# Optimization experiments

Hardware: AMD Instinct MI355X
Metric: run time of the kernel (lower is better)

The kernel has to match this reference:

```python
import jax, jax.numpy as jnp
import numpy as np

N = 50000          # nodes
E = 1600000        # edges (avg degree 32)
NUM_FEAT = 512
HIDDEN = 128
NUM_CLASS = 40
NUM_LAYERS = 4
EPS = 0.3


def setup_inputs() -> dict:
    key = jax.random.key(0)
    ks = jax.random.split(key, 8)
    x = jax.random.normal(ks[0], (N, NUM_FEAT), dtype=jnp.float32)
    edge_index = jax.random.randint(ks[1], (2, E), 0, N, dtype=jnp.int64)
    gain = 1.414  # xavier_normal_(gain=1.414) as in reset_parameters
    W1 = jax.random.normal(ks[2], (HIDDEN, NUM_FEAT), dtype=jnp.float32) * gain * (2.0 / (HIDDEN + NUM_FEAT)) ** 0.5
    b1 = jnp.zeros((HIDDEN,), dtype=jnp.float32)
    W2 = jax.random.normal(ks[3], (NUM_CLASS, HIDDEN), dtype=jnp.float32) * gain * (2.0 / (NUM_CLASS + HIDDEN)) ** 0.5
    b2 = jnp.zeros((NUM_CLASS,), dtype=jnp.float32)
    # FAConv attention vectors: Linear(channels, 1, bias=False) per layer
    att_l = jax.random.normal(ks[4], (NUM_LAYERS, HIDDEN), dtype=jnp.float32) * (2.0 / (1 + HIDDEN)) ** 0.5
    att_r = jax.random.normal(ks[5], (NUM_LAYERS, HIDDEN), dtype=jnp.float32) * (2.0 / (1 + HIDDEN)) ** 0.5
    return dict(x=x, edge_index=edge_index, W1=W1, b1=b1, W2=W2, b2=b2, att_l=att_l, att_r=att_r)


def reference(x, edge_index, W1, b1, W2, b2, att_l, att_r):
    n = x.shape[0]
    # gcn_norm with self-loops (FAConv default add_self_loops=True)
    loops = jnp.arange(n, dtype=edge_index.dtype)
    src = jnp.concatenate([edge_index[0], loops])  # source j
    dst = jnp.concatenate([edge_index[1], loops])  # target i
    deg = jax.ops.segment_sum(jnp.ones_like(src, dtype=x.dtype), dst, num_segments=n)
    dis = jax.lax.rsqrt(jnp.maximum(deg, 1.0))
    norm = dis[src] * dis[dst]  # [E+N]

    # eval mode: dropout is identity
    h = jax.nn.relu(x @ W1.T + b1)  # [N, HIDDEN]
    raw = h
    for l in range(NUM_LAYERS):
        al = h @ att_l[l]  # [N]
        ar = h @ att_r[l]  # [N]
        coef = jnp.tanh(al[src] + ar[dst]) * norm            # [E+N]
        agg = jax.ops.segment_sum(h[src] * coef[:, None], dst, num_segments=n)
        h = agg + EPS * raw
    logits = h @ W2.T + b2  # [N, NUM_CLASS]
    return jax.nn.log_softmax(logits, axis=1)
```

## Files before the change

### kernel.cpp

```cpp
#include <hip/hip_runtime.h>
#include <cmath>


#define HIDDEN 128
#define FEAT 512
#define NCLASS 40
#define LDST 40
#define LDSW 132
#define NB 256
#define PITCH 12544
#define BM1 64

typedef __attribute__((ext_vector_type(8))) short short8;
typedef __attribute__((ext_vector_type(4))) float f32x4;

__device__ __forceinline__ float bf_lo(unsigned u) { return __uint_as_float(u << 16); }
__device__ __forceinline__ float bf_hi(unsigned u) { return __uint_as_float(u & 0xffff0000u); }
__device__ __forceinline__ unsigned pack_bf16(float x, float y) {
    unsigned ux = __float_as_uint(x);
    unsigned uy = __float_as_uint(y);
    unsigned lx = (ux + 0x7fffu + ((ux >> 16) & 1u)) >> 16;
    unsigned hy = (uy + 0x7fffu + ((uy >> 16) & 1u)) & 0xffff0000u;
    return hy | lx;
}
__device__ __forceinline__ float fast_tanh(float x) {
    x = fminf(fmaxf(x, -15.f), 15.f);
    float e = __expf(2.f * x);
    return (e - 1.f) / (e + 1.f);
}

__global__ __launch_bounds__(256) void k_hist(const int* __restrict__ ei, int E, int CE,
                                              unsigned* __restrict__ partial,
                                              ushort* __restrict__ lrank) {
    __shared__ unsigned lh[PITCH];
    const int b = blockIdx.x, tid = threadIdx.x;
    for (int w = tid; w < PITCH; w += 256) lh[w] = 0;
    __syncthreads();
    int e0 = b * CE, e1 = min(E, e0 + CE);
    for (int e = e0 + tid; e < e1; e += 256) {
        int dst = ei[E + e];
        int sh = (dst & 3) * 8;
        unsigned old = atomicAdd(&lh[dst >> 2], 1u << sh);
        lrank[e] = (ushort)((old >> sh) & 0xffu);
    }
    __syncthreads();
    unsigned* prow = partial + (size_t)b * PITCH;
    for (int w = tid; w < PITCH; w += 256) prow[w] = lh[w];
}

__global__ __launch_bounds__(256) void k_hscan(unsigned* __restrict__ partial,
                                               int* __restrict__ deg,
                                               float* __restrict__ dis, int n) {
    int w = blockIdx.x * 256 + threadIdx.x;
    if (w >= PITCH) return;
    unsigned run = 0;
    size_t idx = w;
    for (int b = 0; b < NB; ++b, idx += PITCH) {
        unsigned v = partial[idx];
        partial[idx] = run;
        run += v;
    }
    int node = 4 * w;
    int d0 = run & 0xffu, d1 = (run >> 8) & 0xffu, d2 = (run >> 16) & 0xffu, d3 = run >> 24;
    if (node < n)     { deg[node]     = d0; dis[node]     = rsqrtf((float)(d0 + 1)); }
    if (node + 1 < n) { deg[node + 1] = d1; dis[node + 1] = rsqrtf((float)(d1 + 1)); }
    if (node + 2 < n) { deg[node + 2] = d2; dis[node + 2] = rsqrtf((float)(d2 + 1)); }
    if (node + 3 < n) { deg[node + 3] = d3; dis[node + 3] = rsqrtf((float)(d3 + 1)); }
}

__global__ __launch_bounds__(256) void k_scan1(const int* __restrict__ deg, int* __restrict__ offs,
                                               int* __restrict__ part, int n) {
    __shared__ int s[256];
    int tid = threadIdx.x;
    int gid = blockIdx.x * 256 + tid;
    int v = (gid < n) ? deg[gid] : 0;
    s[tid] = v;
    __syncthreads();
    for (int off = 1; off < 256; off <<= 1) {
        int t = (tid >= off) ? s[tid - off] : 0;
        __syncthreads();
        s[tid] += t;
        __syncthreads();
    }
    if (gid < n) offs[gid] = s[tid] - v;
    if (tid == 255) part[blockIdx.x] = s[255];
}

__global__ __launch_bounds__(256) void k_scan2(int* __restrict__ part, int nb) {
    __shared__ int s[256];
    int tid = threadIdx.x;
    int v = (tid < nb) ? part[tid] : 0;
    s[tid] = v;
    __syncthreads();
    for (int off = 1; off < 256; off <<= 1) {
        int t = (tid >= off) ? s[tid - off] : 0;
        __syncthreads();
        s[tid] += t;
        __syncthreads();
    }
    if (tid < nb) part[tid] = s[tid] - v;
}

__global__ __launch_bounds__(256) void k_scan3(int* __restrict__ offs, const int* __restrict__ part,
                                               int n, int E) {
    int gid = blockIdx.x * 256 + threadIdx.x;
    if (gid < n) offs[gid] += part[blockIdx.x];
    if (gid == 0) offs[n] = E;
}

__global__ __launch_bounds__(256) void k_csr_fill(const int* __restrict__ ei, int E, int CE,
                                                  const int* __restrict__ offs,
                                                  const unsigned* __restrict__ partial,
                                                  const ushort* __restrict__ lrank,
                                                  int* __restrict__ csrc) {
    __shared__ unsigned lp[PITCH];
    const int b = blockIdx.x, tid = threadIdx.x;
    const unsigned* prow = partial + (size_t)b * PITCH;
    for (int w = tid; w < PITCH; w += 256) lp[w] = prow[w];
    __syncthreads();
    int e0 = b * CE, e1 = min(E, e0 + CE);
    for (int e = e0 + tid; e < e1; e += 256) {
        int dst = ei[E + e];
        int src = ei[e];
        unsigned wv = lp[dst >> 2];
        int base = (wv >> ((dst & 3) * 8)) & 0xffu;
        csrc[offs[dst] + base + (int)lrank[e]] = src;
    }
}

__global__ __launch_bounds__(256) void k_gemm1(const float* __restrict__ x,
                                               const float* __restrict__ W1,
                                               const float* __restrict__ b1,
                                               float* __restrict__ h, int M) {
    __shared__ ushort As[BM1 * LDST];
    __shared__ ushort Bs[128 * LDST];
    const int tid = threadIdx.x;
    const int bm = blockIdx.x * BM1;
    const int wave = tid >> 6, lane = tid & 63;
    const int rh = (wave >> 1) * 32;
    const int ch = (wave & 1) * 64;
    const int sub = lane & 15, quad = lane >> 4;
    const int lrow = tid >> 3;
    const int lcol = (tid & 7) * 4;
    f32x4 acc[2][4] = {};
    float4 av[2], bv[4];
#pragma unroll
    for (int i = 0; i < 2; ++i) {
        int grow = bm + lrow + 32 * i;
        av[i] = (grow < M) ? *(const float4*)(x + (size_t)grow * FEAT + lcol)
                           : make_float4(0.f, 0.f, 0.f, 0.f);
    }
#pragma unroll
    for (int i = 0; i < 4; ++i)
        bv[i] = *(const float4*)(W1 + (size_t)(lrow + 32 * i) * FEAT + lcol);

    for (int k0 = 0; k0 < FEAT; k0 += 32) {
#pragma unroll
        for (int i = 0; i < 2; ++i)
            *(uint2*)(As + (lrow + 32 * i) * LDST + lcol) =
                make_uint2(pack_bf16(av[i].x, av[i].y), pack_bf16(av[i].z, av[i].w));
#pragma unroll
        for (int i = 0; i < 4; ++i)
            *(uint2*)(Bs + (lrow + 32 * i) * LDST + lcol) =
                make_uint2(pack_bf16(bv[i].x, bv[i].y), pack_bf16(bv[i].z, bv[i].w));
        __syncthreads();
        if (k0 + 32 < FEAT) {
            const int kn = k0 + 32;
#pragma unroll
            for (int i = 0; i < 2; ++i) {
                int grow = bm + lrow + 32 * i;
                av[i] = (grow < M) ? *(const float4*)(x + (size_t)grow * FEAT + kn + lcol)
                                   : make_float4(0.f, 0.f, 0.f, 0.f);
            }
#pragma unroll
            for (int i = 0; i < 4; ++i)
                bv[i] = *(const float4*)(W1 + (size_t)(lrow + 32 * i) * FEAT + kn + lcol);
        }
        short8 af[2], bfr[4];
#pragma unroll
        for (int t = 0; t < 2; ++t)
            af[t] = *(const short8*)(As + (rh + t * 16 + sub) * LDST + quad * 8);
#pragma unroll
        for (int u = 0; u < 4; ++u)
            bfr[u] = *(const short8*)(Bs + (ch + u * 16 + sub) * LDST + quad * 8);
#pragma unroll
        for (int t = 0; t < 2; ++t)
#pragma unroll
            for (int u = 0; u < 4; ++u)
                acc[t][u] = __builtin_amdgcn_mfma_f32_16x16x32_bf16(af[t], bfr[u], acc[t][u], 0, 0, 0);
        __syncthreads();
    }
    float b1v[4];
#pragma unroll
    for (int u = 0; u < 4; ++u) b1v[u] = b1[ch + u * 16 + sub];
#pragma unroll
    for (int t = 0; t < 2; ++t) {
#pragma unroll
        for (int u = 0; u < 4; ++u) {
            int col = ch + u * 16 + sub;
#pragma unroll
            for (int r2 = 0; r2 < 4; ++r2) {
                int grow = bm + rh + t * 16 + quad * 4 + r2;
                if (grow < M)
                    h[(size_t)grow * HIDDEN + col] = fmaxf(acc[t][u][r2] + b1v[u], 0.f);
            }
        }
    }
}

__global__ __launch_bounds__(256) void k_prep(const float* __restrict__ h, unsigned* __restrict__ hbf,
                       const float* __restrict__ attl, const float* __restrict__ attr,
                       const float* __restrict__ dis, float2* __restrict__ al2,
                       float* __restrict__ ar, int n) {
    int node = (blockIdx.x * blockDim.x + threadIdx.x) >> 6;
    int lane = threadIdx.x & 63;
    if (node >= n) return;
    float2 hv = ((const float2*)(h + (size_t)node * HIDDEN))[lane];
    hbf[(size_t)node * 64 + lane] = pack_bf16(hv.x, hv.y);
    float pl = hv.x * attl[2 * lane] + hv.y * attl[2 * lane + 1];
    float pr = hv.x * attr[2 * lane] + hv.y * attr[2 * lane + 1];
    for (int off = 32; off; off >>= 1) {
        pl += __shfl_down(pl, off);
        pr += __shfl_down(pr, off);
    }
    if (lane == 0) {
        al2[node] = make_float2(pl, dis[node]);
        ar[node] = pr;
    }
}

__global__ __launch_bounds__(256) void k_aggregate(
                            const unsigned* __restrict__ hbf, const float* __restrict__ raw,
                            const float2* __restrict__ al2, const float* __restrict__ ar,
                            const int* __restrict__ offs, const int* __restrict__ csrc,
                            float* __restrict__ hout, unsigned* __restrict__ houtbf,
                            const float* __restrict__ attl_n, const float* __restrict__ attr_n,
                            float2* __restrict__ al2_o, float* __restrict__ ar_o, int n) {
    int node = (blockIdx.x * blockDim.x + threadIdx.x) >> 6;
    int lane = threadIdx.x & 63;
    if (node >= n) return;
    const int grp = lane >> 4;
    const int sub = lane & 15;
    const float arn = ar[node];
    const float2 selfld = al2[node];
    const float disn = selfld.y;
    float acc[8] = {0.f, 0.f, 0.f, 0.f, 0.f, 0.f, 0.f, 0.f};
    int e0 = offs[node], e1 = offs[node + 1];
    for (int base = e0; base < e1; base += 64) {
        int cnt = min(64, e1 - base);
        int idx = base + lane;
        int smy = (lane < cnt) ? csrc[idx] : node;
        float2 lmy = al2[smy];
        float cmy = (lane < cnt) ? fast_tanh(lmy.x + arn) * lmy.y * disn : 0.f;
        int t = 0;
        for (; t + 16 <= cnt; t += 16) {
            int sa = __shfl(smy, t + grp);
            int sb = __shfl(smy, t + 4 + grp);
            int sc = __shfl(smy, t + 8 + grp);
            int sd = __shfl(smy, t + 12 + grp);
            float ca = __shfl(cmy, t + grp);
            float cb = __shfl(cmy, t + 4 + grp);
            float cc = __shfl(cmy, t + 8 + grp);
            float cd = __shfl(cmy, t + 12 + grp);
            uint4 ra = *(const uint4*)(hbf + (size_t)sa * 64 + sub * 4);
            uint4 rb = *(const uint4*)(hbf + (size_t)sb * 64 + sub * 4);
            uint4 rc = *(const uint4*)(hbf + (size_t)sc * 64 + sub * 4);
            uint4 rd = *(const uint4*)(hbf + (size_t)sd * 64 + sub * 4);
            acc[0] += ca * bf_lo(ra.x); acc[1] += ca * bf_hi(ra.x);
            acc[2] += ca * bf_lo(ra.y); acc[3] += ca * bf_hi(ra.y);
            acc[4] += ca * bf_lo(ra.z); acc[5] += ca * bf_hi(ra.z);
            acc[6] += ca * bf_lo(ra.w); acc[7] += ca * bf_hi(ra.w);
            acc[0] += cb * bf_lo(rb.x); acc[1] += cb * bf_hi(rb.x);
            acc[2] += cb * bf_lo(rb.y); acc[3] += cb * bf_hi(rb.y);
            acc[4] += cb * bf_lo(rb.z); acc[5] += cb * bf_hi(rb.z);
            acc[6] += cb * bf_lo(rb.w); acc[7] += cb * bf_hi(rb.w);
            acc[0] += cc * bf_lo(rc.x); acc[1] += cc * bf_hi(rc.x);
            acc[2] += cc * bf_lo(rc.y); acc[3] += cc * bf_hi(rc.y);
            acc[4] += cc * bf_lo(rc.z); acc[5] += cc * bf_hi(rc.z);
            acc[6] += cc * bf_lo(rc.w); acc[7] += cc * bf_hi(rc.w);
            acc[0] += cd * bf_lo(rd.x); acc[1] += cd * bf_hi(rd.x);
            acc[2] += cd * bf_lo(rd.y); acc[3] += cd * bf_hi(rd.y);
            acc[4] += cd * bf_lo(rd.z); acc[5] += cd * bf_hi(rd.z);
            acc[6] += cd * bf_lo(rd.w); acc[7] += cd * bf_hi(rd.w);
        }
        for (; t < cnt; t += 4) {
            int sa = __shfl(smy, t + grp);
            float ca = __shfl(cmy, t + grp);
            uint4 ra = *(const uint4*)(hbf + (size_t)sa * 64 + sub * 4);
            acc[0] += ca * bf_lo(ra.x); acc[1] += ca * bf_hi(ra.x);
            acc[2] += ca * bf_lo(ra.y); acc[3] += ca * bf_hi(ra.y);
            acc[4] += ca * bf_lo(ra.z); acc[5] += ca * bf_hi(ra.z);
            acc[6] += ca * bf_lo(ra.w); acc[7] += ca * bf_hi(ra.w);
        }
    }
#pragma unroll
    for (int j = 0; j < 8; ++j) {
        acc[j] += __shfl_xor(acc[j], 16);
        acc[j] += __shfl_xor(acc[j], 32);
    }
    {
        float c = fast_tanh(selfld.x + arn) * disn * disn;
        uint4 r = *(const uint4*)(hbf + (size_t)node * 64 + sub * 4);
        acc[0] += c * bf_lo(r.x); acc[1] += c * bf_hi(r.x);
        acc[2] += c * bf_lo(r.y); acc[3] += c * bf_hi(r.y);
        acc[4] += c * bf_lo(r.z); acc[5] += c * bf_hi(r.z);
        acc[6] += c * bf_lo(r.w); acc[7] += c * bf_hi(r.w);
    }
    float o[8];
    {
        float4 rv0 = *(const float4*)(raw + (size_t)node * HIDDEN + sub * 8);
        float4 rv1 = *(const float4*)(raw + (size_t)node * HIDDEN + sub * 8 + 4);
        o[0] = acc[0] + 0.3f * rv0.x; o[1] = acc[1] + 0.3f * rv0.y;
        o[2] = acc[2] + 0.3f * rv0.z; o[3] = acc[3] + 0.3f * rv0.w;
        o[4] = acc[4] + 0.3f * rv1.x; o[5] = acc[5] + 0.3f * rv1.y;
        o[6] = acc[6] + 0.3f * rv1.z; o[7] = acc[7] + 0.3f * rv1.w;
    }
    if (grp == 0) {
        *(float4*)(hout + (size_t)node * HIDDEN + sub * 8) = make_float4(o[0], o[1], o[2], o[3]);
        *(float4*)(hout + (size_t)node * HIDDEN + sub * 8 + 4) = make_float4(o[4], o[5], o[6], o[7]);
        if (houtbf) {
            uint4 pk = make_uint4(pack_bf16(o[0], o[1]), pack_bf16(o[2], o[3]),
                                  pack_bf16(o[4], o[5]), pack_bf16(o[6], o[7]));
            *(uint4*)(houtbf + (size_t)node * 64 + sub * 4) = pk;
        }
    }
    if (attl_n) {
        float4 a0 = *(const float4*)(attl_n + sub * 8);
        float4 a1 = *(const float4*)(attl_n + sub * 8 + 4);
        float4 c0 = *(const float4*)(attr_n + sub * 8);
        float4 c1 = *(const float4*)(attr_n + sub * 8 + 4);
        float pl = o[0] * a0.x + o[1] * a0.y + o[2] * a0.z + o[3] * a0.w +
                   o[4] * a1.x + o[5] * a1.y + o[6] * a1.z + o[7] * a1.w;
        float pr = o[0] * c0.x + o[1] * c0.y + o[2] * c0.z + o[3] * c0.w +
                   o[4] * c1.x + o[5] * c1.y + o[6] * c1.z + o[7] * c1.w;
        for (int off = 8; off; off >>= 1) {
            pl += __shfl_xor(pl, off);
            pr += __shfl_xor(pr, off);
        }
        if (lane == 0) {
            al2_o[node] = make_float2(pl, disn);
            ar_o[node] = pr;
        }
    }
}

__global__ __launch_bounds__(256, 4) void k_out(const float* __restrict__ h,
                                                const float* __restrict__ W2,
                                                const float* __restrict__ b2,
                                                float* __restrict__ out, int n) {
    __shared__ float ws[NCLASS * LDSW];
    __shared__ float bs[NCLASS];
    const int tid = threadIdx.x;
    for (int i = tid; i < NCLASS * (HIDDEN / 4); i += 256) {
        int r = i >> 5;
        int c4 = i & 31;
        *(float4*)(ws + r * LDSW + c4 * 4) = ((const float4*)W2)[i];
    }
    if (tid < NCLASS) bs[tid] = b2[tid];
    __syncthreads();
    int node = blockIdx.x * 32 + (tid >> 3);
    const int ol = tid & 7;
    if (node >= n) return;
    const float* hr = h + (size_t)node * HIDDEN;
    float acc[5];
#pragma unroll
    for (int c = 0; c < 5; ++c) acc[c] = bs[ol + 8 * c];
#pragma unroll
    for (int k0 = 0; k0 < HIDDEN; k0 += 16) {
        float4 h0 = *(const float4*)(hr + k0);
        float4 h1 = *(const float4*)(hr + k0 + 4);
        float4 h2v = *(const float4*)(hr + k0 + 8);
        float4 h3 = *(const float4*)(hr + k0 + 12);
#pragma unroll
        for (int c = 0; c < 5; ++c) {
            const float* w = ws + (ol + 8 * c) * LDSW + k0;
            float4 w0 = *(const float4*)(w);
            float4 w1 = *(const float4*)(w + 4);
            float4 w2v = *(const float4*)(w + 8);
            float4 w3 = *(const float4*)(w + 12);
            acc[c] += h0.x * w0.x + h0.y * w0.y + h0.z * w0.z + h0.w * w0.w +
                      h1.x * w1.x + h1.y * w1.y + h1.z * w1.z + h1.w * w1.w +
                      h2v.x * w2v.x + h2v.y * w2v.y + h2v.z * w2v.z + h2v.w * w2v.w +
                      h3.x * w3.x + h3.y * w3.y + h3.z * w3.z + h3.w * w3.w;
        }
    }
    float m = acc[0];
#pragma unroll
    for (int c = 1; c < 5; ++c) m = fmaxf(m, acc[c]);
    m = fmaxf(m, __shfl_xor(m, 1));
    m = fmaxf(m, __shfl_xor(m, 2));
    m = fmaxf(m, __shfl_xor(m, 4));
    float ssum = 0.f;
#pragma unroll
    for (int c = 0; c < 5; ++c) ssum += expf(acc[c] - m);
    ssum += __shfl_xor(ssum, 1);
    ssum += __shfl_xor(ssum, 2);
    ssum += __shfl_xor(ssum, 4);
    float lse = m + logf(ssum);
    float* orow = out + (size_t)node * NCLASS;
#pragma unroll
    for (int c = 0; c < 5; ++c) orow[ol + 8 * c] = acc[c] - lse;
}

extern "C" void kernel_launch(void* const* d_in, const int* in_sizes, int n_in,
                              void* d_out, int out_size, void* d_ws, size_t ws_size,
                              hipStream_t stream) {
    const float* x    = (const float*)d_in[0];
    const int*   ei   = (const int*)d_in[1];
    const float* W1   = (const float*)d_in[2];
    const float* b1   = (const float*)d_in[3];
    const float* W2   = (const float*)d_in[4];
    const float* b2   = (const float*)d_in[5];
    const float* attl = (const float*)d_in[6];
    const float* attr = (const float*)d_in[7];
    const int N = in_sizes[0] / FEAT;
    const int E = in_sizes[1] / 2;
    float* out = (float*)d_out;

    char* p = (char*)d_ws;
    auto take = [&](size_t bytes) {
        void* q = (void*)p;
        p += (bytes + 255) & ~(size_t)255;
        return q;
    };
    float*    h0   = (float*)take((size_t)N * HIDDEN * 4);
    float*    h1   = (float*)take((size_t)N * HIDDEN * 4);
    float*    h2   = (float*)take((size_t)N * HIDDEN * 4);
    unsigned* hb0  = (unsigned*)take((size_t)N * 64 * 4);
    unsigned* hb1  = (unsigned*)take((size_t)N * 64 * 4);
    int*      deg  = (int*)take((size_t)N * 4);
    float*    dis  = (float*)take((size_t)N * 4);
    int*      offs = (int*)take((size_t)(N + 1) * 4);
    unsigned* partial = (unsigned*)take((size_t)NB * PITCH * 4);
    ushort*   lrank   = (ushort*)take((size_t)E * 2);
    int*      csrc = (int*)take((size_t)E * 4);
    float2*   al2A = (float2*)take((size_t)N * 8);
    float2*   al2B = (float2*)take((size_t)N * 8);
    float*    arA  = (float*)take((size_t)N * 4);
    float*    arB  = (float*)take((size_t)N * 4);
    int*      part = (int*)take(1024);

    const int nbl = (N + 255) / 256;
    const int CE = (E + NB - 1) / NB;

    k_hist<<<NB, 256, 0, stream>>>(ei, E, CE, partial, lrank);
    k_hscan<<<(PITCH + 255) / 256, 256, 0, stream>>>(partial, deg, dis, N);
    k_scan1<<<nbl, 256, 0, stream>>>(deg, offs, part, N);
    k_scan2<<<1, 256, 0, stream>>>(part, nbl);
    k_scan3<<<nbl, 256, 0, stream>>>(offs, part, N, E);
    k_csr_fill<<<NB, 256, 0, stream>>>(ei, E, CE, offs, partial, lrank, csrc);

    k_gemm1<<<(N + BM1 - 1) / BM1, 256, 0, stream>>>(x, W1, b1, h0, N);
    k_prep<<<(N + 3) / 4, 256, 0, stream>>>(h0, hb0, attl, attr, dis, al2A, arA, N);

    float*    fout[4] = {h1, h2, h1, h2};
    unsigned* hbin = hb0, *hbout = hb1;
    float2*   alin = al2A, *alout = al2B;
    float*    arin = arA,  *arout = arB;
    for (int l = 0; l < 4; ++l) {
        const float* attl_n = (l < 3) ? (attl + (l + 1) * HIDDEN) : nullptr;
        const float* attr_n = (l < 3) ? (attr + (l + 1) * HIDDEN) : nullptr;
        unsigned* hbo = (l < 3) ? hbout : nullptr;
        k_aggregate<<<(N + 3) / 4, 256, 0, stream>>>(hbin, h0, alin, arin, offs, csrc,
                                                     fout[l], hbo, attl_n, attr_n,
                                                     alout, arout, N);
        unsigned* tb = hbin; hbin = hbout; hbout = tb;
        float2* ta = alin; alin = alout; alout = ta;
        float* tr = arin; arin = arout; arout = tr;
    }

    k_out<<<(N + 31) / 32, 256, 0, stream>>>(h2, W2, b2, out, N);
}
```

Measured before the change: 523.0 us.

## Replace LDS-histogram CSR build with global-atomic counting sort

Drops the per-block shared-memory histogram with packed 8-bit counters, the partial-sum column scan and the rank array. In their place it counts degrees with global atomics, scans them, and fills the CSR by atomically bumping a per-node cursor. This removes the large partial buffer traffic and the serial 256-step column scan, but adds contention on global atomics. Neighbor order within each row is no longer deterministic, which can change the floating-point summation order.

```diff
diff --git a/kernel.cpp b/kernel.cpp
--- a/kernel.cpp
+++ b/kernel.cpp
@@ -7,8 +7,6 @@
 #define NCLASS 40
 #define LDST 40
 #define LDSW 132
-#define NB 256
-#define PITCH 12544
 #define BM1 64
 
 typedef __attribute__((ext_vector_type(8))) short short8;
@@ -29,43 +27,10 @@
     return (e - 1.f) / (e + 1.f);
 }
 
-__global__ __launch_bounds__(256) void k_hist(const int* __restrict__ ei, int E, int CE,
-                                              unsigned* __restrict__ partial,
-                                              ushort* __restrict__ lrank) {
-    __shared__ unsigned lh[PITCH];
-    const int b = blockIdx.x, tid = threadIdx.x;
-    for (int w = tid; w < PITCH; w += 256) lh[w] = 0;
-    __syncthreads();
-    int e0 = b * CE, e1 = min(E, e0 + CE);
-    for (int e = e0 + tid; e < e1; e += 256) {
-        int dst = ei[E + e];
-        int sh = (dst & 3) * 8;
-        unsigned old = atomicAdd(&lh[dst >> 2], 1u << sh);
-        lrank[e] = (ushort)((old >> sh) & 0xffu);
-    }
-    __syncthreads();
-    unsigned* prow = partial + (size_t)b * PITCH;
-    for (int w = tid; w < PITCH; w += 256) prow[w] = lh[w];
-}
-
-__global__ __launch_bounds__(256) void k_hscan(unsigned* __restrict__ partial,
-                                               int* __restrict__ deg,
-                                               float* __restrict__ dis, int n) {
-    int w = blockIdx.x * 256 + threadIdx.x;
-    if (w >= PITCH) return;
-    unsigned run = 0;
-    size_t idx = w;
-    for (int b = 0; b < NB; ++b, idx += PITCH) {
-        unsigned v = partial[idx];
-        partial[idx] = run;
-        run += v;
-    }
-    int node = 4 * w;
-    int d0 = run & 0xffu, d1 = (run >> 8) & 0xffu, d2 = (run >> 16) & 0xffu, d3 = run >> 24;
-    if (node < n)     { deg[node]     = d0; dis[node]     = rsqrtf((float)(d0 + 1)); }
-    if (node + 1 < n) { deg[node + 1] = d1; dis[node + 1] = rsqrtf((float)(d1 + 1)); }
-    if (node + 2 < n) { deg[node + 2] = d2; dis[node + 2] = rsqrtf((float)(d2 + 1)); }
-    if (node + 3 < n) { deg[node + 3] = d3; dis[node + 3] = rsqrtf((float)(d3 + 1)); }
+__global__ __launch_bounds__(256) void k_deg(const int* __restrict__ ei, int E,
+                                             int* __restrict__ deg) {
+    int e = blockIdx.x * 256 + threadIdx.x;
+    if (e < E) atomicAdd(&deg[ei[E + e]], 1);
 }
 
 __global__ __launch_bounds__(256) void k_scan1(const int* __restrict__ deg, int* __restrict__ offs,
@@ -102,29 +67,27 @@
 }
 
 __global__ __launch_bounds__(256) void k_scan3(int* __restrict__ offs, const int* __restrict__ part,
+                                               int* __restrict__ cur, float* __restrict__ dis,
                                                int n, int E) {
     int gid = blockIdx.x * 256 + threadIdx.x;
-    if (gid < n) offs[gid] += part[blockIdx.x];
+    if (gid < n) {
+        int d = cur[gid];
+        int o = offs[gid] + part[blockIdx.x];
+        offs[gid] = o;
+        cur[gid] = o;
+        dis[gid] = rsqrtf((float)(d + 1));
+    }
     if (gid == 0) offs[n] = E;
 }
 
-__global__ __launch_bounds__(256) void k_csr_fill(const int* __restrict__ ei, int E, int CE,
-                                                  const int* __restrict__ offs,
-                                                  const unsigned* __restrict__ partial,
-                                                  const ushort* __restrict__ lrank,
-                                                  int* __restrict__ csrc) {
-    __shared__ unsigned lp[PITCH];
-    const int b = blockIdx.x, tid = threadIdx.x;
-    const unsigned* prow = partial + (size_t)b * PITCH;
-    for (int w = tid; w < PITCH; w += 256) lp[w] = prow[w];
-    __syncthreads();
-    int e0 = b * CE, e1 = min(E, e0 + CE);
-    for (int e = e0 + tid; e < e1; e += 256) {
+__global__ __launch_bounds__(256) void k_fill(const int* __restrict__ ei, int E,
+                                              int* __restrict__ cur, int* __restrict__ csrc) {
+    int e = blockIdx.x * 256 + threadIdx.x;
+    if (e < E) {
         int dst = ei[E + e];
         int src = ei[e];
-        unsigned wv = lp[dst >> 2];
-        int base = (wv >> ((dst & 3) * 8)) & 0xffu;
-        csrc[offs[dst] + base + (int)lrank[e]] = src;
+        int pos = atomicAdd(&cur[dst], 1);
+        csrc[pos] = src;
     }
 }
 
@@ -431,8 +394,6 @@
     int*      deg  = (int*)take((size_t)N * 4);
     float*    dis  = (float*)take((size_t)N * 4);
     int*      offs = (int*)take((size_t)(N + 1) * 4);
-    unsigned* partial = (unsigned*)take((size_t)NB * PITCH * 4);
-    ushort*   lrank   = (ushort*)take((size_t)E * 2);
     int*      csrc = (int*)take((size_t)E * 4);
     float2*   al2A = (float2*)take((size_t)N * 8);
     float2*   al2B = (float2*)take((size_t)N * 8);
@@ -441,14 +402,14 @@
     int*      part = (int*)take(1024);
 
     const int nbl = (N + 255) / 256;
-    const int CE = (E + NB - 1) / NB;
-
-    k_hist<<<NB, 256, 0, stream>>>(ei, E, CE, partial, lrank);
-    k_hscan<<<(PITCH + 255) / 256, 256, 0, stream>>>(partial, deg, dis, N);
+    const int ebl = (E + 255) / 256;
+
+    hipMemsetAsync(deg, 0, (size_t)N * 4, stream);
+    k_deg<<<ebl, 256, 0, stream>>>(ei, E, deg);
     k_scan1<<<nbl, 256, 0, stream>>>(deg, offs, part, N);
     k_scan2<<<1, 256, 0, stream>>>(part, nbl);
-    k_scan3<<<nbl, 256, 0, stream>>>(offs, part, N, E);
-    k_csr_fill<<<NB, 256, 0, stream>>>(ei, E, CE, offs, partial, lrank, csrc);
+    k_scan3<<<nbl, 256, 0, stream>>>(offs, part, deg, dis, N, E);
+    k_fill<<<ebl, 256, 0, stream>>>(ei, E, deg, csrc);
 
     k_gemm1<<<(N + BM1 - 1) / BM1, 256, 0, stream>>>(x, W1, b1, h0, N);
     k_prep<<<(N + 3) / 4, 256, 0, stream>>>(h0, hb0, attl, attr, dis, al2A, arA, N);
```

New measurement: 646.3 us. 1.24x slower.
